# Kernel tuning notes

Hardware: AMD Instinct MI355X
Metric: run time of the kernel (lower is better)

## Reference

```python
import jax, jax.numpy as jnp
import numpy as np

NK, NT, NC, NM = 2048, 512, 32, 512
NOISE_SCALE = 0.001


def _nac(x, w_hat, m_hat):
    # NeuralAccumulatorCell: W = tanh(W_hat) * sigmoid(M_hat); y = x @ W.T
    w = jnp.tanh(w_hat) * jax.nn.sigmoid(m_hat)
    return x @ w.T


def setup_inputs() -> dict:
    key = jax.random.key(0)
    ks = jax.random.split(key, 21)
    def p(k, out_f, in_f):
        return (jax.random.normal(k, (out_f, in_f), jnp.float32)
                / np.sqrt(in_f).astype(np.float32))
    inp = {
        "X": jax.random.normal(ks[0], (NK, NT, NC), jnp.float32),
        "noise": jax.random.normal(ks[1], (NK, NC), jnp.float32),
        # ch_zip: Nac(nC,nC), Nac(nC,1)
        "wz1": p(ks[2], NC, NC), "mz1": p(ks[3], NC, NC),
        "wz2": p(ks[4], 1, NC),  "mz2": p(ks[5], 1, NC),
        # ch_unzip: Nac(1,nC)
        "wu": p(ks[6], NC, 1),   "mu": p(ks[7], NC, 1),
        # t_zip: Nac(nT,nM), Nac(nM,nM), Nac(nM,nM)
        "wt1": p(ks[8], NM, NT), "mt1": p(ks[9], NM, NT),
        "wt2": p(ks[10], NM, NM), "mt2": p(ks[11], NM, NM),
        "wt3": p(ks[12], NM, NM), "mt3": p(ks[13], NM, NM),
        # delta_M: Nac(nM,nM), Nac(nM,nM), Nac(nM,1)
        "wd1": p(ks[14], NM, NM), "md1": p(ks[15], NM, NM),
        "wd2": p(ks[16], NM, NM), "md2": p(ks[17], NM, NM),
        "wd3": p(ks[18], 1, NM),  "md3": p(ks[19], 1, NM),
    }
    return inp


def reference(X, noise, wz1, mz1, wz2, mz2, wu, mu,
              wt1, mt1, wt2, mt2, wt3, mt3,
              wd1, md1, wd2, md2, wd3, md3):
    # ch_zip over every (k,t) channel vector -> scalar: (K,T,C) -> (K,T)
    uni_y = _nac(_nac(X, wz1, mz1), wz2, mz2)[..., 0]
    # t_zip per k: (K,T) -> (K,NM)
    mem_y = _nac(_nac(_nac(uni_y, wt1, mt1), wt2, mt2), wt3, mt3)
    # delta_M: (K,NM) -> (K,1)
    delta_uni = _nac(_nac(_nac(mem_y, wd1, md1), wd2, md2), wd3, md3)
    # ch_unzip: (K,1) -> (K,C)
    delta_mv = _nac(delta_uni, wu, mu)
    lastX = X[:, -1, :]                                   # (K,C)
    baseline = lastX - lastX.mean(axis=-1, keepdims=True)
    y = delta_mv + baseline + baseline * (noise * NOISE_SCALE)
    return y
```

## Files before the change

### kernel.cpp

```cpp
#include <hip/hip_runtime.h>
#include <math.h>

#define NK 2048
#define NT 512
#define NC 32
#define NM 512
#define NCHAIN 32
#define NBLK 1024
#define NUNI (NBLK - NCHAIN)
#define MAGICV 0x13579BDFu
#define POISON 0xAAAAAAAAu
#define CTR_DONE (POISON + (unsigned)NCHAIN)

#define R_OFF   0
#define CTR_OFF (5 * NM)
#define MIR_OFF (CTR_OFF + 5 * 16)

__device__ __forceinline__ float eff_w(float w, float m) {
    const float t = 1.f - 2.f / (__expf(2.f * w) + 1.f);
    const float s = 1.f / (1.f + __expf(-m));
    return t * s;
}

__device__ __forceinline__ float cp_load(const float* p) {
    return __hip_atomic_load(p, __ATOMIC_RELAXED, __HIP_MEMORY_SCOPE_AGENT);
}

__global__ __launch_bounds__(256, 4) void fused_kernel(
    const float* __restrict__ X,   const float* __restrict__ noise,
    const float* __restrict__ wz1, const float* __restrict__ mz1,
    const float* __restrict__ wz2, const float* __restrict__ mz2,
    const float* __restrict__ wu,  const float* __restrict__ mu,
    const float* __restrict__ wt1, const float* __restrict__ mt1,
    const float* __restrict__ wt2, const float* __restrict__ mt2,
    const float* __restrict__ wt3, const float* __restrict__ mt3,
    const float* __restrict__ wd1, const float* __restrict__ md1,
    const float* __restrict__ wd2, const float* __restrict__ md2,
    const float* __restrict__ wd3, const float* __restrict__ md3,
    float* __restrict__ out, float* __restrict__ ws)
{
    __shared__ float W1s[NC * NC];
    __shared__ float W2s[NC];
    __shared__ float vl[NC], ul[NC];
    __shared__ float unirow[3][NT];
    __shared__ float lastr[3][NC];
    __shared__ float gl[NM];
    __shared__ float rl[NM];
    __shared__ float4 part[2][128];
    __shared__ float wred[4];

    const int tid = threadIdx.x;
    const int b   = blockIdx.x;
    unsigned* U   = (unsigned*)ws;

    if (b < NCHAIN) {
        for (int e = tid; e < NM; e += 256) rl[e] = eff_w(wd3[e], md3[e]);
        __syncthreads();

        const float* Ws[5] = {wd2, wd1, wt3, wt2, wt1};
        const float* Ms[5] = {md2, md1, mt3, mt2, mt1};

        const int j4   = (tid & 127) * 4;
        const int half = tid >> 7;

        #pragma unroll
        for (int l = 0; l < 5; ++l) {
            const float* __restrict__ w = Ws[l];
            const float* __restrict__ m = Ms[l];
            float ax = 0.f, ay = 0.f, az = 0.f, aw = 0.f;
            #pragma unroll
            for (int s = 0; s < 8; ++s) {
                const int i = b * 16 + half * 8 + s;
                const float ri = rl[i];
                const float4 wv = *(const float4*)(w + (size_t)i * NM + j4);
                const float4 mv = *(const float4*)(m + (size_t)i * NM + j4);
                ax += ri * eff_w(wv.x, mv.x);
                ay += ri * eff_w(wv.y, mv.y);
                az += ri * eff_w(wv.z, mv.z);
                aw += ri * eff_w(wv.w, mv.w);
            }
            part[half][tid & 127] = make_float4(ax, ay, az, aw);
            __syncthreads();

            float* dst = ws + R_OFF + (size_t)l * NM;
            if (tid < 128) {
                const float4 a = part[0][tid], c = part[1][tid];
                atomicAdd(dst + tid * 4 + 0, a.x + c.x);
                atomicAdd(dst + tid * 4 + 1, a.y + c.y);
                atomicAdd(dst + tid * 4 + 2, a.z + c.z);
                atomicAdd(dst + tid * 4 + 3, a.w + c.w);
            }
            __syncthreads();

            unsigned* ctr = &U[CTR_OFF + l * 16];
            if (tid == 0) {
                atomicAdd(ctr, 1u);
                while (atomicAdd(ctr, 0u) != CTR_DONE) __builtin_amdgcn_s_sleep(2);
            }
            __syncthreads();

            if (l < 4) {
                rl[tid]       = cp_load(dst + tid);
                rl[tid + 256] = cp_load(dst + tid + 256);
                __syncthreads();
            }
        }

        if (tid == 0) {
            #pragma unroll
            for (int s = 0; s < 256; s += NCHAIN)
                atomicExch(&U[MIR_OFF + (s + b) * 16], MAGICV);
        }
        return;
    }

    const int u  = b - NCHAIN;
    const int nk = (u < NK - 2 * NUNI) ? 3 : 2;

    for (int e = tid; e < NC * NC; e += 256) W1s[e] = eff_w(wz1[e], mz1[e]);
    if (tid < NC) W2s[tid] = eff_w(wz2[tid], mz2[tid]);
    __syncthreads();
    if (tid < NC) {
        float a = 0.f;
        #pragma unroll
        for (int j = 0; j < NC; ++j) a += W2s[j] * W1s[j * NC + tid];
        vl[tid] = a;
        ul[tid] = eff_w(wu[tid], mu[tid]);
    }
    __syncthreads();

    const int c = (tid * 4) & 31;
    const float v0 = vl[c], v1 = vl[c + 1], v2 = vl[c + 2], v3 = vl[c + 3];

    for (int rep = 0; rep < nk; ++rep) {
        const int k = u + rep * NUNI;
        const float4* __restrict__ Xk = (const float4*)(X + (size_t)k * (NT * NC));
        #pragma unroll
        for (int it = 0; it < 16; ++it) {
            const float4 x = Xk[tid + it * 256];
            float p = x.x * v0 + x.y * v1 + x.z * v2 + x.w * v3;
            p += __shfl_xor(p, 1);
            p += __shfl_xor(p, 2);
            p += __shfl_xor(p, 4);
            if ((tid & 7) == 0) unirow[rep][(tid >> 3) + it * 32] = p;
        }
        if (tid < NC)
            lastr[rep][tid] = X[(size_t)k * (NT * NC) + (size_t)(NT - 1) * NC + tid];
    }

    if (tid == 0) {
        unsigned* mir = &U[MIR_OFF + (u & 255) * 16];
        while (atomicAdd(mir, 0u) != MAGICV) __builtin_amdgcn_s_sleep(16);
    }
    __syncthreads();

    gl[tid]       = cp_load(ws + R_OFF + 4 * NM + tid);
    gl[tid + 256] = cp_load(ws + R_OFF + 4 * NM + tid + 256);
    __syncthreads();

    for (int rep = 0; rep < nk; ++rep) {
        const int k = u + rep * NUNI;
        float d = unirow[rep][tid] * gl[tid] + unirow[rep][tid + 256] * gl[tid + 256];
        #pragma unroll
        for (int off = 32; off > 0; off >>= 1) d += __shfl_xor(d, off);
        if ((tid & 63) == 0) wred[tid >> 6] = d;
        __syncthreads();
        if (tid < NC) {
            const float delta = wred[0] + wred[1] + wred[2] + wred[3];
            const float lx = lastr[rep][tid];
            float s = lx;
            s += __shfl_xor(s, 1);
            s += __shfl_xor(s, 2);
            s += __shfl_xor(s, 4);
            s += __shfl_xor(s, 8);
            s += __shfl_xor(s, 16);
            const float bse = lx - s * (1.0f / NC);
            const float n = noise[k * NC + tid];
            out[k * NC + tid] = delta * ul[tid] + bse * (1.0f + 0.001f * n);
        }
        __syncthreads();
    }
}

extern "C" void kernel_launch(void* const* d_in, const int* in_sizes, int n_in,
                              void* d_out, int out_size, void* d_ws, size_t ws_size,
                              hipStream_t stream)
{
    const float* X     = (const float*)d_in[0];
    const float* noise = (const float*)d_in[1];
    const float* wz1   = (const float*)d_in[2];
    const float* mz1   = (const float*)d_in[3];
    const float* wz2   = (const float*)d_in[4];
    const float* mz2   = (const float*)d_in[5];
    const float* wu    = (const float*)d_in[6];
    const float* mu    = (const float*)d_in[7];
    const float* wt1   = (const float*)d_in[8];
    const float* mt1   = (const float*)d_in[9];
    const float* wt2   = (const float*)d_in[10];
    const float* mt2   = (const float*)d_in[11];
    const float* wt3   = (const float*)d_in[12];
    const float* mt3   = (const float*)d_in[13];
    const float* wd1   = (const float*)d_in[14];
    const float* md1   = (const float*)d_in[15];
    const float* wd2   = (const float*)d_in[16];
    const float* md2   = (const float*)d_in[17];
    const float* wd3   = (const float*)d_in[18];
    const float* md3   = (const float*)d_in[19];
    float* out = (float*)d_out;
    float* ws  = (float*)d_ws;

    fused_kernel<<<NBLK, 256, 0, stream>>>(
        X, noise, wz1, mz1, wz2, mz2, wu, mu,
        wt1, mt1, wt2, mt2, wt3, mt3,
        wd1, md1, wd2, md2, wd3, md3, out, ws);
}
```

Measured before the change: 243.3 us.

## Split fused kernel into chain kernel and per-row streaming kernel

```diff
diff --git a/kernel.cpp b/kernel.cpp
--- a/kernel.cpp
+++ b/kernel.cpp
@@ -6,15 +6,11 @@
 #define NC 32
 #define NM 512
 #define NCHAIN 32
-#define NBLK 1024
-#define NUNI (NBLK - NCHAIN)
-#define MAGICV 0x13579BDFu
 #define POISON 0xAAAAAAAAu
 #define CTR_DONE (POISON + (unsigned)NCHAIN)
 
-#define R_OFF   0
+#define ACC_OFF 0
 #define CTR_OFF (5 * NM)
-#define MIR_OFF (CTR_OFF + 5 * 16)
 
 __device__ __forceinline__ float eff_w(float w, float m) {
     const float t = 1.f - 2.f / (__expf(2.f * w) + 1.f);
@@ -26,96 +22,93 @@
     return __hip_atomic_load(p, __ATOMIC_RELAXED, __HIP_MEMORY_SCOPE_AGENT);
 }
 
-__global__ __launch_bounds__(256, 4) void fused_kernel(
-    const float* __restrict__ X,   const float* __restrict__ noise,
-    const float* __restrict__ wz1, const float* __restrict__ mz1,
-    const float* __restrict__ wz2, const float* __restrict__ mz2,
-    const float* __restrict__ wu,  const float* __restrict__ mu,
+__global__ __launch_bounds__(256) void chain_kernel(
     const float* __restrict__ wt1, const float* __restrict__ mt1,
     const float* __restrict__ wt2, const float* __restrict__ mt2,
     const float* __restrict__ wt3, const float* __restrict__ mt3,
     const float* __restrict__ wd1, const float* __restrict__ md1,
     const float* __restrict__ wd2, const float* __restrict__ md2,
     const float* __restrict__ wd3, const float* __restrict__ md3,
-    float* __restrict__ out, float* __restrict__ ws)
+    float* __restrict__ ws)
 {
-    __shared__ float W1s[NC * NC];
-    __shared__ float W2s[NC];
-    __shared__ float vl[NC], ul[NC];
-    __shared__ float unirow[3][NT];
-    __shared__ float lastr[3][NC];
-    __shared__ float gl[NM];
-    __shared__ float rl[NM];
+    __shared__ float rin[16];
     __shared__ float4 part[2][128];
-    __shared__ float wred[4];
 
     const int tid = threadIdx.x;
     const int b   = blockIdx.x;
     unsigned* U   = (unsigned*)ws;
 
-    if (b < NCHAIN) {
-        for (int e = tid; e < NM; e += 256) rl[e] = eff_w(wd3[e], md3[e]);
+    if (tid < 16) rin[tid] = eff_w(wd3[b * 16 + tid], md3[b * 16 + tid]);
+    __syncthreads();
+
+    const float* Ws[5] = {wd2, wd1, wt3, wt2, wt1};
+    const float* Ms[5] = {md2, md1, mt3, mt2, mt1};
+
+    const int j4   = (tid & 127) * 4;
+    const int half = tid >> 7;
+
+    #pragma unroll
+    for (int l = 0; l < 5; ++l) {
+        const float* __restrict__ w = Ws[l];
+        const float* __restrict__ m = Ms[l];
+        float ax = 0.f, ay = 0.f, az = 0.f, aw = 0.f;
+        #pragma unroll
+        for (int s = 0; s < 8; ++s) {
+            const int i = b * 16 + half * 8 + s;
+            const float ri = rin[half * 8 + s];
+            const float4 wv = *(const float4*)(w + (size_t)i * NM + j4);
+            const float4 mv = *(const float4*)(m + (size_t)i * NM + j4);
+            ax += ri * eff_w(wv.x, mv.x);
+            ay += ri * eff_w(wv.y, mv.y);
+            az += ri * eff_w(wv.z, mv.z);
+            aw += ri * eff_w(wv.w, mv.w);
+        }
+        part[half][tid & 127] = make_float4(ax, ay, az, aw);
         __syncthreads();
 
-        const float* Ws[5] = {wd2, wd1, wt3, wt2, wt1};
-        const float* Ms[5] = {md2, md1, mt3, mt2, mt1};
+        float* acc = ws + ACC_OFF + (size_t)l * NM;
+        if (tid < 128) {
+            const float4 a = part[0][tid], c = part[1][tid];
+            atomicAdd(acc + tid * 4 + 0, a.x + c.x);
+            atomicAdd(acc + tid * 4 + 1, a.y + c.y);
+            atomicAdd(acc + tid * 4 + 2, a.z + c.z);
+            atomicAdd(acc + tid * 4 + 3, a.w + c.w);
+        }
+        __syncthreads();
 
-        const int j4   = (tid & 127) * 4;
-        const int half = tid >> 7;
-
-        #pragma unroll
-        for (int l = 0; l < 5; ++l) {
-            const float* __restrict__ w = Ws[l];
-            const float* __restrict__ m = Ms[l];
-            float ax = 0.f, ay = 0.f, az = 0.f, aw = 0.f;
-            #pragma unroll
-            for (int s = 0; s < 8; ++s) {
-                const int i = b * 16 + half * 8 + s;
-                const float ri = rl[i];
-                const float4 wv = *(const float4*)(w + (size_t)i * NM + j4);
-                const float4 mv = *(const float4*)(m + (size_t)i * NM + j4);
-                ax += ri * eff_w(wv.x, mv.x);
-                ay += ri * eff_w(wv.y, mv.y);
-                az += ri * eff_w(wv.z, mv.z);
-                aw += ri * eff_w(wv.w, mv.w);
-            }
-            part[half][tid & 127] = make_float4(ax, ay, az, aw);
-            __syncthreads();
-
-            float* dst = ws + R_OFF + (size_t)l * NM;
-            if (tid < 128) {
-                const float4 a = part[0][tid], c = part[1][tid];
-                atomicAdd(dst + tid * 4 + 0, a.x + c.x);
-                atomicAdd(dst + tid * 4 + 1, a.y + c.y);
-                atomicAdd(dst + tid * 4 + 2, a.z + c.z);
-                atomicAdd(dst + tid * 4 + 3, a.w + c.w);
-            }
-            __syncthreads();
-
+        if (l < 4) {
             unsigned* ctr = &U[CTR_OFF + l * 16];
             if (tid == 0) {
                 atomicAdd(ctr, 1u);
                 while (atomicAdd(ctr, 0u) != CTR_DONE) __builtin_amdgcn_s_sleep(2);
             }
             __syncthreads();
+            if (tid < 16) rin[tid] = cp_load(acc + b * 16 + tid);
+            __syncthreads();
+        }
+    }
+}
 
-            if (l < 4) {
-                rl[tid]       = cp_load(dst + tid);
-                rl[tid + 256] = cp_load(dst + tid + 256);
-                __syncthreads();
-            }
-        }
+__global__ __launch_bounds__(256) void stream_kernel(
+    const float* __restrict__ X,   const float* __restrict__ noise,
+    const float* __restrict__ wz1, const float* __restrict__ mz1,
+    const float* __restrict__ wz2, const float* __restrict__ mz2,
+    const float* __restrict__ wu,  const float* __restrict__ mu,
+    float* __restrict__ out, const float* __restrict__ ws)
+{
+    __shared__ float W1s[NC * NC];
+    __shared__ float W2s[NC];
+    __shared__ float vl[NC], ul[NC];
+    __shared__ float gl[NM];
+    __shared__ float unirow[NT];
+    __shared__ float lastx[NC];
+    __shared__ float wred[4];
 
-        if (tid == 0) {
-            #pragma unroll
-            for (int s = 0; s < 256; s += NCHAIN)
-                atomicExch(&U[MIR_OFF + (s + b) * 16], MAGICV);
-        }
-        return;
-    }
+    const int tid = threadIdx.x;
+    const int k   = blockIdx.x;
 
-    const int u  = b - NCHAIN;
-    const int nk = (u < NK - 2 * NUNI) ? 3 : 2;
+    gl[tid]       = ws[ACC_OFF + 4 * NM + tid];
+    gl[tid + 256] = ws[ACC_OFF + 4 * NM + tid + 256];
 
     for (int e = tid; e < NC * NC; e += 256) W1s[e] = eff_w(wz1[e], mz1[e]);
     if (tid < NC) W2s[tid] = eff_w(wz2[tid], mz2[tid]);
@@ -132,53 +125,38 @@
     const int c = (tid * 4) & 31;
     const float v0 = vl[c], v1 = vl[c + 1], v2 = vl[c + 2], v3 = vl[c + 3];
 
-    for (int rep = 0; rep < nk; ++rep) {
-        const int k = u + rep * NUNI;
-        const float4* __restrict__ Xk = (const float4*)(X + (size_t)k * (NT * NC));
-        #pragma unroll
-        for (int it = 0; it < 16; ++it) {
-            const float4 x = Xk[tid + it * 256];
-            float p = x.x * v0 + x.y * v1 + x.z * v2 + x.w * v3;
-            p += __shfl_xor(p, 1);
-            p += __shfl_xor(p, 2);
-            p += __shfl_xor(p, 4);
-            if ((tid & 7) == 0) unirow[rep][(tid >> 3) + it * 32] = p;
-        }
-        if (tid < NC)
-            lastr[rep][tid] = X[(size_t)k * (NT * NC) + (size_t)(NT - 1) * NC + tid];
+    const float4* __restrict__ Xk = (const float4*)(X + (size_t)k * (NT * NC));
+    #pragma unroll
+    for (int it = 0; it < 16; ++it) {
+        const float4 x = Xk[tid + it * 256];
+        float p = x.x * v0 + x.y * v1 + x.z * v2 + x.w * v3;
+        p += __shfl_xor(p, 1);
+        p += __shfl_xor(p, 2);
+        p += __shfl_xor(p, 4);
+        if ((tid & 7) == 0) unirow[(tid >> 3) + it * 32] = p;
     }
-
-    if (tid == 0) {
-        unsigned* mir = &U[MIR_OFF + (u & 255) * 16];
-        while (atomicAdd(mir, 0u) != MAGICV) __builtin_amdgcn_s_sleep(16);
-    }
+    if (tid < NC)
+        lastx[tid] = X[(size_t)k * (NT * NC) + (size_t)(NT - 1) * NC + tid];
     __syncthreads();
 
-    gl[tid]       = cp_load(ws + R_OFF + 4 * NM + tid);
-    gl[tid + 256] = cp_load(ws + R_OFF + 4 * NM + tid + 256);
+    float d = unirow[tid] * gl[tid] + unirow[tid + 256] * gl[tid + 256];
+    #pragma unroll
+    for (int off = 32; off > 0; off >>= 1) d += __shfl_xor(d, off);
+    if ((tid & 63) == 0) wred[tid >> 6] = d;
     __syncthreads();
 
-    for (int rep = 0; rep < nk; ++rep) {
-        const int k = u + rep * NUNI;
-        float d = unirow[rep][tid] * gl[tid] + unirow[rep][tid + 256] * gl[tid + 256];
-        #pragma unroll
-        for (int off = 32; off > 0; off >>= 1) d += __shfl_xor(d, off);
-        if ((tid & 63) == 0) wred[tid >> 6] = d;
-        __syncthreads();
-        if (tid < NC) {
-            const float delta = wred[0] + wred[1] + wred[2] + wred[3];
-            const float lx = lastr[rep][tid];
-            float s = lx;
-            s += __shfl_xor(s, 1);
-            s += __shfl_xor(s, 2);
-            s += __shfl_xor(s, 4);
-            s += __shfl_xor(s, 8);
-            s += __shfl_xor(s, 16);
-            const float bse = lx - s * (1.0f / NC);
-            const float n = noise[k * NC + tid];
-            out[k * NC + tid] = delta * ul[tid] + bse * (1.0f + 0.001f * n);
-        }
-        __syncthreads();
+    if (tid < NC) {
+        const float delta = wred[0] + wred[1] + wred[2] + wred[3];
+        const float lx = lastx[tid];
+        float s = lx;
+        s += __shfl_xor(s, 1);
+        s += __shfl_xor(s, 2);
+        s += __shfl_xor(s, 4);
+        s += __shfl_xor(s, 8);
+        s += __shfl_xor(s, 16);
+        const float bse = lx - s * (1.0f / NC);
+        const float n = noise[k * NC + tid];
+        out[k * NC + tid] = delta * ul[tid] + bse * (1.0f + 0.001f * n);
     }
 }
 
@@ -209,8 +187,9 @@
     float* out = (float*)d_out;
     float* ws  = (float*)d_ws;
 
-    fused_kernel<<<NBLK, 256, 0, stream>>>(
-        X, noise, wz1, mz1, wz2, mz2, wu, mu,
+    chain_kernel<<<NCHAIN, 256, 0, stream>>>(
         wt1, mt1, wt2, mt2, wt3, mt3,
-        wd1, md1, wd2, md2, wd3, md3, out, ws);
+        wd1, md1, wd2, md2, wd3, md3, ws);
+    stream_kernel<<<NK, 256, 0, stream>>>(
+        X, noise, wz1, mz1, wz2, mz2, wu, mu, out, ws);
 }
```

Result: slower. 263.0 us (+8.1%).
